# Kernel optimization log

Measured on AMD Instinct MI355X. Metric: run time of the kernel, lower is better.

## Reference

```python
import jax, jax.numpy as jnp
import numpy as np

N_NODES = 100000


def gcn_conv(x, src, dst, W, b):
    # x: [N, F_in]; src/dst: [E'] (self-loops already appended)
    n = x.shape[0]
    deg = jax.ops.segment_sum(jnp.ones_like(src, dtype=x.dtype), dst, num_segments=n)
    dinv = jnp.where(deg > 0, jax.lax.rsqrt(deg), 0.0)
    norm = dinv[src] * dinv[dst]                      # [E']
    h = x @ W                                         # [N, F_out] (GEMM first: F_out small)
    msg = h[src] * norm[:, None]                      # gather + scale
    out = jax.ops.segment_sum(msg, dst, num_segments=n)  # scatter-add
    return out + b


def setup_inputs() -> dict:
    key = jax.random.key(0)
    k1, k2, k3, k4 = jax.random.split(key, 4)
    x = jax.random.normal(k1, (N_NODES, 1433), dtype=jnp.float32)
    edge_index = jax.random.randint(k2, (2, 3200000), 0, N_NODES, dtype=jnp.int32)
    W1 = jax.random.normal(k3, (1433, 32), dtype=jnp.float32) * (1.0 / np.sqrt(1433.0))
    b1 = jnp.zeros((32,), dtype=jnp.float32)
    W2 = jax.random.normal(k4, (32, 7), dtype=jnp.float32) * (1.0 / np.sqrt(32.0))
    b2 = jnp.zeros((7,), dtype=jnp.float32)
    return {"x": x, "edge_index": edge_index, "W1": W1, "b1": b1, "W2": W2, "b2": b2}


def reference(x, edge_index, W1, b1, W2, b2):
    n = x.shape[0]
    loop = jnp.arange(n, dtype=edge_index.dtype)      # add self-loops (GCNConv default)
    src = jnp.concatenate([edge_index[0], loop])
    dst = jnp.concatenate([edge_index[1], loop])
    h = gcn_conv(x, src, dst, W1, b1)
    h = jax.nn.relu(h)
    # F.dropout with training=False (eval mode) is identity
    h = gcn_conv(h, src, dst, W2, b2)
    return jax.nn.log_softmax(h, axis=1)
```

## Files before the change

kernel.cpp:

```cpp
#include <hip/hip_runtime.h>
#include <math.h>

#define F0 1433
#define F1 32
#define F2 7

__global__ void k_init_deg(float* __restrict__ deg, int N) {
    int i = blockIdx.x * 256 + threadIdx.x;
    if (i < N) deg[i] = 1.0f;
}

__global__ void k_count_deg(const int* __restrict__ dst, float* __restrict__ deg, int E) {
    int e = blockIdx.x * 256 + threadIdx.x;
    if (e < E) atomicAdd(&deg[dst[e]], 1.0f);
}

__global__ void k_dinv(float* __restrict__ deg, int N) {
    int i = blockIdx.x * 256 + threadIdx.x;
    if (i < N) deg[i] = rsqrtf(deg[i]);
}

#define BM 128
#define BK 64
#define XS_LD 68

#define STAGE_LOAD(K0)                                                       \
    {                                                                        \
        const int gk = (K0) + j;                                             \
        const bool kok = gk < F0;                                            \
        const float* xp = x + (long)(row0 + i0) * F0 + gk;                   \
        if (rowfull) {                                                       \
            _Pragma("unroll")                                                \
            for (int l = 0; l < 32; ++l)                                     \
                px[l] = kok ? xp[(long)(4 * l) * F0] : 0.f;                  \
        } else {                                                             \
            _Pragma("unroll")                                                \
            for (int l = 0; l < 32; ++l) {                                   \
                int gr = row0 + i0 + 4 * l;                                  \
                px[l] = (gr < N && kok) ? xp[(long)(4 * l) * F0] : 0.f;      \
            }                                                                \
        }                                                                    \
        _Pragma("unroll")                                                    \
        for (int l = 0; l < 8; ++l) {                                        \
            int idx = tid + l * 256;                                         \
            int gkw = (K0) + (idx >> 5);                                     \
            pw[l] = (gkw < F0) ? W[gkw * F1 + (idx & 31)] : 0.f;             \
        }                                                                    \
    }

#define STAGE_WRITE()                                                        \
    {                                                                        \
        _Pragma("unroll")                                                    \
        for (int l = 0; l < 32; ++l) xs[(i0 + 4 * l) * XS_LD + j] = px[l];   \
        _Pragma("unroll")                                                    \
        for (int l = 0; l < 8; ++l) wsm[tid + l * 256] = pw[l];              \
    }

#define COMPUTE()                                                            \
    _Pragma("unroll")                                                        \
    for (int kk = 0; kk < BK; kk += 4) {                                     \
        float4 x0 = *(const float4*)&xs[(r     ) * XS_LD + kk];              \
        float4 x1 = *(const float4*)&xs[(r + 32) * XS_LD + kk];              \
        float4 x2 = *(const float4*)&xs[(r + 64) * XS_LD + kk];              \
        float4 x3 = *(const float4*)&xs[(r + 96) * XS_LD + kk];              \
        const float a0[4] = {x0.x, x0.y, x0.z, x0.w};                        \
        const float a1[4] = {x1.x, x1.y, x1.z, x1.w};                        \
        const float a2[4] = {x2.x, x2.y, x2.z, x2.w};                        \
        const float a3[4] = {x3.x, x3.y, x3.z, x3.w};                        \
        _Pragma("unroll")                                                    \
        for (int u = 0; u < 4; ++u) {                                        \
            float4 w = *(const float4*)&wsm[(kk + u) * F1 + cg * 4];         \
            acc[0][0] += a0[u] * w.x; acc[0][1] += a0[u] * w.y;              \
            acc[0][2] += a0[u] * w.z; acc[0][3] += a0[u] * w.w;              \
            acc[1][0] += a1[u] * w.x; acc[1][1] += a1[u] * w.y;              \
            acc[1][2] += a1[u] * w.z; acc[1][3] += a1[u] * w.w;              \
            acc[2][0] += a2[u] * w.x; acc[2][1] += a2[u] * w.y;              \
            acc[2][2] += a2[u] * w.z; acc[2][3] += a2[u] * w.w;              \
            acc[3][0] += a3[u] * w.x; acc[3][1] += a3[u] * w.y;              \
            acc[3][2] += a3[u] * w.z; acc[3][3] += a3[u] * w.w;              \
        }                                                                    \
    }

__global__ __launch_bounds__(256, 3) void k_gemm1(const float* __restrict__ x,
                                                  const float* __restrict__ W,
                                                  const float* __restrict__ dinv,
                                                  float* __restrict__ h,
                                                  float* __restrict__ agg, int N) {
    __shared__ float xs[BM * XS_LD];
    __shared__ float wsm[BK * F1];
    const int tid  = threadIdx.x;
    const int row0 = blockIdx.x * BM;
    const int cg   = tid & 7;
    const int r    = tid >> 3;
    const int j    = tid & 63;
    const int i0   = tid >> 6;
    const bool rowfull = (row0 + BM <= N);

    float acc[4][4] = {{0.f, 0.f, 0.f, 0.f}, {0.f, 0.f, 0.f, 0.f},
                       {0.f, 0.f, 0.f, 0.f}, {0.f, 0.f, 0.f, 0.f}};
    float px[32];
    float pw[8];

    STAGE_LOAD(0)
    STAGE_WRITE()
    __syncthreads();

    const int nt = (F0 + BK - 1) / BK;
    for (int t = 0; t < nt - 1; ++t) {
        STAGE_LOAD((t + 1) * BK)
        COMPUTE()
        __syncthreads();
        STAGE_WRITE()
        __syncthreads();
    }
    COMPUTE()

    #pragma unroll
    for (int m = 0; m < 4; ++m) {
        int gr = row0 + r + 32 * m;
        if (gr < N) {
            float4 o = make_float4(acc[m][0], acc[m][1], acc[m][2], acc[m][3]);
            *(float4*)&h[(long)gr * F1 + cg * 4] = o;
            float d = dinv[gr];
            float dd = d * d;
            *(float4*)&agg[(long)gr * F1 + cg * 4] =
                make_float4(o.x * dd, o.y * dd, o.z * dd, o.w * dd);
        }
    }
}

__global__ void k_scatter1(const int* __restrict__ src, const int* __restrict__ dst,
                           const float* __restrict__ dinv, const float* __restrict__ h1,
                           float* __restrict__ agg, int E) {
    int t = blockIdx.x * 256 + threadIdx.x;
    int e = t >> 5;
    if (e >= E) return;
    int f = t & 31;
    int s = src[e], d = dst[e];
    float w = dinv[s] * dinv[d];
    atomicAdd(&agg[d * F1 + f], h1[s * F1 + f] * w);
}

__global__ __launch_bounds__(256) void k_layer2(const float* __restrict__ agg1,
                                                const float* __restrict__ b1,
                                                const float* __restrict__ W2,
                                                const float* __restrict__ dinv,
                                                float* __restrict__ h2,
                                                float* __restrict__ out, int N) {
    __shared__ float w2s[F1 * F2];
    __shared__ float b1s[F1];
    int tid = threadIdx.x;
    if (tid < F1 * F2) w2s[tid] = W2[tid];
    if (tid < F1) b1s[tid] = b1[tid];
    __syncthreads();
    int i = blockIdx.x * 256 + tid;
    if (i >= N) return;
    float v[F1];
    #pragma unroll
    for (int u = 0; u < 8; ++u) {
        float4 t = *(const float4*)&agg1[(long)i * F1 + u * 4];
        v[u*4+0] = fmaxf(t.x + b1s[u*4+0], 0.f);
        v[u*4+1] = fmaxf(t.y + b1s[u*4+1], 0.f);
        v[u*4+2] = fmaxf(t.z + b1s[u*4+2], 0.f);
        v[u*4+3] = fmaxf(t.w + b1s[u*4+3], 0.f);
    }
    float o[F2] = {0.f, 0.f, 0.f, 0.f, 0.f, 0.f, 0.f};
    #pragma unroll
    for (int k = 0; k < F1; ++k) {
        float a = v[k];
        #pragma unroll
        for (int c = 0; c < F2; ++c) o[c] += a * w2s[k * F2 + c];
    }
    float di = dinv[i];
    float dd = di * di;
    #pragma unroll
    for (int c = 0; c < F2; ++c) {
        h2[(long)i * F2 + c] = o[c];
        out[(long)i * F2 + c] = o[c] * dd;
    }
}

__global__ void k_scatter2(const int* __restrict__ src, const int* __restrict__ dst,
                           const float* __restrict__ dinv, const float* __restrict__ h2,
                           float* __restrict__ out, int E) {
    int t = blockIdx.x * 256 + threadIdx.x;
    int e = t >> 3;
    int c = t & 7;
    if (e >= E || c >= F2) return;
    int s = src[e], d = dst[e];
    float w = dinv[s] * dinv[d];
    atomicAdd(&out[(long)d * F2 + c], h2[(long)s * F2 + c] * w);
}

__global__ void k_logsoftmax(float* __restrict__ out, const float* __restrict__ b2, int N) {
    int i = blockIdx.x * 256 + threadIdx.x;
    if (i >= N) return;
    float v[F2];
    float m = -1e30f;
    #pragma unroll
    for (int c = 0; c < F2; ++c) {
        v[c] = out[(long)i * F2 + c] + b2[c];
        m = fmaxf(m, v[c]);
    }
    float s = 0.f;
    #pragma unroll
    for (int c = 0; c < F2; ++c) s += expf(v[c] - m);
    float l = logf(s);
    #pragma unroll
    for (int c = 0; c < F2; ++c) out[(long)i * F2 + c] = v[c] - m - l;
}

extern "C" void kernel_launch(void* const* d_in, const int* in_sizes, int n_in,
                              void* d_out, int out_size, void* d_ws, size_t ws_size,
                              hipStream_t stream) {
    const float* x  = (const float*)d_in[0];
    const int*   ei = (const int*)d_in[1];
    const float* W1 = (const float*)d_in[2];
    const float* b1 = (const float*)d_in[3];
    const float* W2 = (const float*)d_in[4];
    const float* b2 = (const float*)d_in[5];
    float* out = (float*)d_out;

    const int N = in_sizes[0] / F0;
    const int E = in_sizes[1] / 2;
    const int* src = ei;
    const int* dst = ei + E;

    float* ws   = (float*)d_ws;
    size_t o    = 0;
    float* dinv = ws;        o += (size_t)((N + 3) & ~3);
    float* h1   = ws + o;    o += (size_t)N * F1;
    float* agg1 = ws + o;    o += (size_t)N * F1;
    float* h2   = h1;

    const int nb_N  = (N + 255) / 256;
    const int nb_E  = (E + 255) / 256;

    k_init_deg  <<<nb_N, 256, 0, stream>>>(dinv, N);
    k_count_deg <<<nb_E, 256, 0, stream>>>(dst, dinv, E);
    k_dinv      <<<nb_N, 256, 0, stream>>>(dinv, N);

    k_gemm1     <<<(N + BM - 1) / BM, 256, 0, stream>>>(x, W1, dinv, h1, agg1, N);

    k_scatter1  <<<((size_t)E * 32 + 255) / 256, 256, 0, stream>>>(src, dst, dinv, h1, agg1, E);

    k_layer2    <<<nb_N, 256, 0, stream>>>(agg1, b1, W2, dinv, h2, out, N);

    k_scatter2  <<<((size_t)E * 8 + 255) / 256, 256, 0, stream>>>(src, dst, dinv, h2, out, E);

    k_logsoftmax<<<nb_N, 256, 0, stream>>>(out, b2, N);
}
```

Measured before the change: 1.877 ms.

## Load GEMM tiles directly into LDS with global_load_lds and XOR swizzle

```diff
diff --git a/kernel.cpp b/kernel.cpp
--- a/kernel.cpp
+++ b/kernel.cpp
@@ -22,47 +22,24 @@
 
 #define BM 128
 #define BK 64
-#define XS_LD 68
-
-#define STAGE_LOAD(K0)                                                       \
-    {                                                                        \
-        const int gk = (K0) + j;                                             \
-        const bool kok = gk < F0;                                            \
-        const float* xp = x + (long)(row0 + i0) * F0 + gk;                   \
-        if (rowfull) {                                                       \
-            _Pragma("unroll")                                                \
-            for (int l = 0; l < 32; ++l)                                     \
-                px[l] = kok ? xp[(long)(4 * l) * F0] : 0.f;                  \
-        } else {                                                             \
-            _Pragma("unroll")                                                \
-            for (int l = 0; l < 32; ++l) {                                   \
-                int gr = row0 + i0 + 4 * l;                                  \
-                px[l] = (gr < N && kok) ? xp[(long)(4 * l) * F0] : 0.f;      \
-            }                                                                \
-        }                                                                    \
-        _Pragma("unroll")                                                    \
-        for (int l = 0; l < 8; ++l) {                                        \
-            int idx = tid + l * 256;                                         \
-            int gkw = (K0) + (idx >> 5);                                     \
-            pw[l] = (gkw < F0) ? W[gkw * F1 + (idx & 31)] : 0.f;             \
-        }                                                                    \
-    }
-
-#define STAGE_WRITE()                                                        \
-    {                                                                        \
-        _Pragma("unroll")                                                    \
-        for (int l = 0; l < 32; ++l) xs[(i0 + 4 * l) * XS_LD + j] = px[l];   \
-        _Pragma("unroll")                                                    \
-        for (int l = 0; l < 8; ++l) wsm[tid + l * 256] = pw[l];              \
-    }
+#define NT_FULL 22
+#define KTAIL 1408
+
+typedef const __attribute__((address_space(1))) void* gas_ptr;
+typedef __attribute__((address_space(3))) void* las_ptr;
+
+__device__ __forceinline__ void gl_lds4(const void* g, void* l) {
+    __builtin_amdgcn_global_load_lds((gas_ptr)g, (las_ptr)l, 4, 0, 0);
+}
 
 #define COMPUTE()                                                            \
     _Pragma("unroll")                                                        \
     for (int kk = 0; kk < BK; kk += 4) {                                     \
-        float4 x0 = *(const float4*)&xs[(r     ) * XS_LD + kk];              \
-        float4 x1 = *(const float4*)&xs[(r + 32) * XS_LD + kk];              \
-        float4 x2 = *(const float4*)&xs[(r + 64) * XS_LD + kk];              \
-        float4 x3 = *(const float4*)&xs[(r + 96) * XS_LD + kk];              \
+        const int xo = (((kk >> 2) ^ key) << 2);                             \
+        float4 x0 = *(const float4*)&xs[(r     ) * BK + xo];                 \
+        float4 x1 = *(const float4*)&xs[(r + 32) * BK + xo];                 \
+        float4 x2 = *(const float4*)&xs[(r + 64) * BK + xo];                 \
+        float4 x3 = *(const float4*)&xs[(r + 96) * BK + xo];                 \
         const float a0[4] = {x0.x, x0.y, x0.z, x0.w};                        \
         const float a1[4] = {x1.x, x1.y, x1.z, x1.w};                        \
         const float a2[4] = {x2.x, x2.y, x2.z, x2.w};                        \
@@ -81,49 +58,89 @@
         }                                                                    \
     }
 
-__global__ __launch_bounds__(256, 3) void k_gemm1(const float* __restrict__ x,
-                                                  const float* __restrict__ W,
-                                                  const float* __restrict__ dinv,
-                                                  float* __restrict__ h,
-                                                  float* __restrict__ agg, int N) {
-    __shared__ float xs[BM * XS_LD];
+__global__ __launch_bounds__(256) void k_gemm1(const float* __restrict__ x,
+                                               const float* __restrict__ W,
+                                               const float* __restrict__ dinv,
+                                               float* __restrict__ h,
+                                               float* __restrict__ agg, int N) {
+    __shared__ float xs[BM * BK];
     __shared__ float wsm[BK * F1];
     const int tid  = threadIdx.x;
+    const int lane = tid & 63;
+    const int wv   = tid >> 6;
     const int row0 = blockIdx.x * BM;
     const int cg   = tid & 7;
     const int r    = tid >> 3;
-    const int j    = tid & 63;
-    const int i0   = tid >> 6;
+    const int key  = r & 7;
     const bool rowfull = (row0 + BM <= N);
+
+    int lo[8];
+    #pragma unroll
+    for (int q = 0; q < 8; ++q)
+        lo[q] = (((lane >> 2) ^ q) << 2) | (lane & 3);
 
     float acc[4][4] = {{0.f, 0.f, 0.f, 0.f}, {0.f, 0.f, 0.f, 0.f},
                        {0.f, 0.f, 0.f, 0.f}, {0.f, 0.f, 0.f, 0.f}};
-    float px[32];
-    float pw[8];
-
-    STAGE_LOAD(0)
-    STAGE_WRITE()
+
+    for (int t = 0; t < NT_FULL; ++t) {
+        const int k0 = t * BK;
+        __syncthreads();
+        if (rowfull) {
+            const float* xb = x + (size_t)(row0 + wv * 32) * F0 + k0;
+            #pragma unroll
+            for (int it = 0; it < 32; ++it)
+                gl_lds4(xb + (size_t)it * F0 + lo[it & 7],
+                        xs + (wv * 32 + it) * BK);
+        } else {
+            #pragma unroll
+            for (int it = 0; it < 32; ++it) {
+                int gr = row0 + wv * 32 + it;
+                if (gr > N - 1) gr = N - 1;
+                gl_lds4(x + (size_t)gr * F0 + k0 + lo[it & 7],
+                        xs + (wv * 32 + it) * BK);
+            }
+        }
+        {
+            const float* wb = W + (size_t)k0 * F1 + wv * 512 + lane;
+            #pragma unroll
+            for (int it = 0; it < 8; ++it)
+                gl_lds4(wb + it * 64, wsm + wv * 512 + it * 64);
+        }
+        __syncthreads();
+        COMPUTE();
+    }
+
     __syncthreads();
-
-    const int nt = (F0 + BK - 1) / BK;
-    for (int t = 0; t < nt - 1; ++t) {
-        STAGE_LOAD((t + 1) * BK)
-        COMPUTE()
-        __syncthreads();
-        STAGE_WRITE()
-        __syncthreads();
-    }
-    COMPUTE()
+    {
+        const int j = lane;
+        const int i0 = wv;
+        #pragma unroll
+        for (int l = 0; l < 32; ++l) {
+            int row = i0 + 4 * l;
+            int gr = row0 + row;
+            int gk = KTAIL + j;
+            float v = (gr < N && gk < F0) ? x[(size_t)gr * F0 + gk] : 0.f;
+            xs[row * BK + ((((j >> 2) ^ (row & 7)) << 2) | (j & 3))] = v;
+        }
+        #pragma unroll
+        for (int l = 0; l < 8; ++l) {
+            int idx = tid + l * 256;
+            int gk = KTAIL + (idx >> 5);
+            wsm[idx] = (gk < F0) ? W[gk * F1 + (idx & 31)] : 0.f;
+        }
+    }
+    __syncthreads();
+    COMPUTE();
 
     #pragma unroll
     for (int m = 0; m < 4; ++m) {
         int gr = row0 + r + 32 * m;
         if (gr < N) {
             float4 o = make_float4(acc[m][0], acc[m][1], acc[m][2], acc[m][3]);
-            *(float4*)&h[(long)gr * F1 + cg * 4] = o;
+            *(float4*)&h[(size_t)gr * F1 + cg * 4] = o;
             float d = dinv[gr];
             float dd = d * d;
-            *(float4*)&agg[(long)gr * F1 + cg * 4] =
+            *(float4*)&agg[(size_t)gr * F1 + cg * 4] =
                 make_float4(o.x * dd, o.y * dd, o.z * dd, o.w * dd);
         }
     }
```

Measured after the change: 1.669 ms. 11.1% less time.
